# Kernel tuning notes

Hardware: AMD Instinct MI355X
Metric: run time of the kernel (lower is better)

Reference implementation:

```python
import jax, jax.numpy as jnp
import numpy as np

NUM_CLASSES = 80
TOPK = 100
EPS = 1e-6


def _conv(x, w, b, pad):
    y = jax.lax.conv_general_dilated(
        x, w, window_strides=(1, 1), padding=[(pad, pad), (pad, pad)],
        dimension_numbers=('NCHW', 'OIHW', 'NCHW'))
    return y + b[None, :, None, None]


def _seek_local_maximum(p):
    # 8-neighbor local-maximum test with zero padding, plus >= EPS threshold.
    pp = jnp.pad(p, ((0, 0), (0, 0), (1, 1), (1, 1)))
    m = ((p >= pp[:, :, :-2, 1:-1]) & (p >= pp[:, :, 2:, 1:-1]) &
         (p >= pp[:, :, 1:-1, :-2]) & (p >= pp[:, :, 1:-1, 2:]) &
         (p >= pp[:, :, :-2, :-2]) & (p >= pp[:, :, :-2, 2:]) &
         (p >= pp[:, :, 2:, :-2]) & (p >= pp[:, :, 2:, 2:]) &
         (p >= EPS))
    return m.astype(p.dtype)


def setup_inputs() -> dict:
    key = jax.random.key(0)
    k = jax.random.split(key, 4)
    B, C, H, W = 8, 256, 128, 128
    return {
        'x': jax.random.normal(k[0], (B, C, H, W), jnp.float32),
        'pos_embeddings': jax.random.normal(k[1], (1, C, H, W), jnp.float32),
        'w1': jax.random.normal(k[2], (C, C, 3, 3), jnp.float32) * 0.02,
        'b1': jnp.zeros((C,), jnp.float32),
        'w2': jax.random.normal(k[3], (NUM_CLASSES + 1, C, 1, 1), jnp.float32) * 0.02,
        'b2': jnp.zeros((NUM_CLASSES + 1,), jnp.float32),
    }


def reference(x, pos_embeddings, w1, b1, w2, b2):
    b, c, h, w = x.shape
    # conv3x3 -> relu -> conv1x1 class logits  [b, num_classes+1, h, w]
    logits = _conv(jax.nn.relu(_conv(x, w1, b1, 1)), w2, b2, 0)
    probs = jax.nn.softmax(logits, axis=1)
    # keep only the winning foreground class per pixel (one-hot mask)
    cls_idx = jnp.argmax(probs[:, :NUM_CLASSES], axis=1)  # [b, h, w]
    one_hot = jax.nn.one_hot(cls_idx, NUM_CLASSES + 1, dtype=probs.dtype)
    probs = probs * jnp.transpose(one_hot, (0, 3, 1, 2))
    # boost local maxima (unrolled NMS) then topk over best-class score map
    probs = probs + _seek_local_maximum(probs)
    scores = jnp.max(probs[:, :NUM_CLASSES], axis=1).reshape(b, h * w)
    _, idx = jax.lax.top_k(scores, TOPK)  # [b, TOPK]
    topk_proposals = jnp.take_along_axis(
        x.reshape(b, c, h * w), idx[:, None, :], axis=2)
    pe = jnp.broadcast_to(pos_embeddings, (b,) + pos_embeddings.shape[1:])
    topk_pos_embeddings = jnp.take_along_axis(
        pe.reshape(b, -1, h * w), idx[:, None, :], axis=2)
    # eval mode: topk_locations is None in the original; omit it here
    return topk_proposals, topk_pos_embeddings, logits
```

## Files before the change

### kernel.cpp

```cpp
#include <hip/hip_runtime.h>
#include <cmath>

#define BATCH 8
#define CHN 256
#define HH 128
#define WW 128
#define HWSZ (HH*WW)
#define NCLS 81
#define NFG 80
#define KTOP 100
#define EPSV 1e-6f

typedef __attribute__((ext_vector_type(8))) short short8;
typedef __attribute__((ext_vector_type(4))) float f32x4;

__device__ __forceinline__ ushort f2bf(float f) {
    unsigned u = __float_as_uint(f);
    return (ushort)((u + 0x7FFFu + ((u >> 16) & 1u)) >> 16);
}
__device__ __forceinline__ float bf2f(ushort h) {
    return __uint_as_float(((unsigned)h) << 16);
}

__device__ __forceinline__ void gl16(const void* g, void* l) {
    __builtin_amdgcn_global_load_lds(
        (const __attribute__((address_space(1))) void*)g,
        (__attribute__((address_space(3))) void*)l, 16, 0, 0);
}

__global__ __launch_bounds__(256) void prep_x(
    const float* __restrict__ x, ushort* __restrict__ xh, ushort* __restrict__ xl)
{
    __shared__ float tile[32 * 321];
    const int blk = blockIdx.x;
    const int q4 = blk & 3, h = (blk >> 2) & 127, b = blk >> 9;
    const int w0 = q4 << 5;
    const int t = threadIdx.x;
    const int px1 = t & 31, cq = t >> 5;

    const float* xb = x + ((size_t)b * CHN) * HWSZ + h * WW + w0;
#pragma unroll 4
    for (int i = 0; i < 32; ++i) {
        tile[px1 * 321 + i * 10 + cq] = xb[(size_t)(i * 8 + cq) * HWSZ + px1];
    }
    __syncthreads();
    for (int i = 0; i < 4; ++i) {
        int u = i * 256 + t;
        int c8 = u & 31, px = u >> 5;
        short8 hv, lv;
#pragma unroll
        for (int j = 0; j < 8; ++j) {
            float f = tile[px * 321 + c8 * 10 + j];
            ushort hb = f2bf(f);
            hv[j] = (short)hb;
            lv[j] = (short)f2bf(f - bf2f(hb));
        }
        size_t addr = ((size_t)b * HWSZ + h * WW + w0 + px) * CHN + c8 * 8;
        *(short8*)(xh + addr) = hv;
        *(short8*)(xl + addr) = lv;
    }
}

__global__ __launch_bounds__(256) void prep_w(
    const float* __restrict__ w1, const float* __restrict__ w2,
    ushort* __restrict__ Bsw, ushort* __restrict__ w2sw)
{
    int i = blockIdx.x * 256 + threadIdx.x;
    if (i < 73728) {
        int tap  = i >> 13;
        int rem  = i & 8191;
        int kt   = rem >> 10;
        int rem2 = rem & 1023;
        int ntg  = rem2 >> 6;
        int lane = rem2 & 63;
        int oc   = ntg * 16 + (lane & 15);
        int ic0  = kt * 32 + (lane >> 4) * 8;
        size_t base = (size_t)(tap * 8 + kt) * 16384 + (size_t)ntg * 512 + lane * 8;
#pragma unroll
        for (int j = 0; j < 8; ++j) {
            float w  = w1[(size_t)oc * 2304 + (ic0 + j) * 9 + tap];
            ushort hb = f2bf(w);
            Bsw[base + j]        = hb;
            Bsw[base + 8192 + j] = f2bf(w - bf2f(hb));
        }
    } else {
        int j2 = i - 73728;
        int kt   = j2 / 768;
        int rem  = j2 - kt * 768;
        int spl  = rem / 384;
        int rem2 = rem - spl * 384;
        int ntg  = rem2 >> 6;
        int lane = rem2 & 63;
        int oc   = ntg * 16 + (lane & 15);
        int ic0  = kt * 32 + (lane >> 4) * 8;
        size_t base = (size_t)(kt * 12 + spl * 6 + ntg) * 512 + lane * 8;
#pragma unroll
        for (int j = 0; j < 8; ++j) {
            float w = (oc < NCLS) ? w2[(size_t)oc * CHN + ic0 + j] : 0.f;
            ushort hb = f2bf(w);
            w2sw[base + j] = spl ? f2bf(w - bf2f(hb)) : hb;
        }
    }
}

__global__ __launch_bounds__(256, 2) void conv3_pipe(
    const ushort* __restrict__ xh, const ushort* __restrict__ xl,
    const ushort* __restrict__ Bsw, const float* __restrict__ b1,
    float* __restrict__ y)
{
    __shared__ ushort A[3][2][132 * 32];

    const int blk  = blockIdx.x;
    const int b    = blk & 7;
    const int h    = blk >> 3;
    const int t    = threadIdx.x;
    const int lane = t & 63;
    const int w    = t >> 6;
    const int l15  = lane & 15;
    const int q    = lane >> 4;

    int colb[4], basew[4];
#pragma unroll
    for (int r = 0; r < 4; ++r) {
        int e   = (r * 256 + t) & 511;
        int pxs = (e >> 2) + 1;
        int qq  = e & 3;
        int qs  = qq ^ ((pxs >> 1) & 3);
        colb[r]  = (pxs - 1) * CHN + qs * 8;
        basew[r] = ((((r * 256 + (t & 192)) & 511) >> 2) + 1) * 32;
    }

    const short8 zz = {0, 0, 0, 0, 0, 0, 0, 0};
    f32x4 acc[8][4];
#pragma unroll
    for (int i = 0; i < 8; ++i)
#pragma unroll
        for (int j = 0; j < 4; ++j) { f32x4 z = {0.f, 0.f, 0.f, 0.f}; acc[i][j] = z; }

    if (t < 96) {
        int sl = t >> 5, rr = t & 31, arr = rr >> 4, pp = (rr >> 2) & 3, qq = rr & 3;
        int pxs = pp ? 128 + pp : 0;
        *(short8*)&A[sl][arr][pxs * 32 + qq * 8] = zz;
    }
    if (h == 0 || h == 127) {
        const int sl = (h == 0) ? 0 : 2;
        for (int u = t; u < 1056; u += 256) {
            int arr = u >= 528; int v = arr ? u - 528 : u;
            *(short8*)&A[sl][arr][v * 8] = zz;
        }
    }

    auto stage = [&](int sn) {
        int kt1 = sn / 3;
        int kh1 = sn - kt1 * 3;
        int gh  = h - 1 + kh1;
        if ((unsigned)gh < (unsigned)HH) {
            size_t rowb = ((size_t)(b * HH + gh) * WW) * CHN + kt1 * 32;
#pragma unroll
            for (int r = 0; r < 4; ++r) {
                const ushort* g = (r < 2 ? xh : xl) + rowb + colb[r];
                gl16(g, &A[kh1][r >> 1][basew[r]]);
            }
        }
    };

    stage(0);
    stage(1);

#pragma unroll 1
    for (int s = 0; s < 24; ++s) {
        const int kt = s / 3;
        const int kh = s - kt * 3;
        {
            const int kh1n = (s + 1) % 3;
            const bool nx4 = (s < 23) &&
                !((h == 0 && kh1n == 0) || (h == 127 && kh1n == 2));
            if (nx4) asm volatile("s_waitcnt vmcnt(4) lgkmcnt(0)" ::: "memory");
            else     asm volatile("s_waitcnt vmcnt(0) lgkmcnt(0)" ::: "memory");
            __builtin_amdgcn_s_barrier();
            __builtin_amdgcn_sched_barrier(0);
        }
#pragma unroll
        for (int kw = 0; kw < 3; ++kw) {
            const int tap = kh * 3 + kw;
            const ushort* bk = Bsw + (size_t)(tap * 8 + kt) * 16384 + lane * 8;
            short8 bh[4], bl[4];
#pragma unroll
            for (int nt = 0; nt < 4; ++nt) {
                bh[nt] = *(const short8*)(bk + (w * 4 + nt) * 512);
                bl[nt] = *(const short8*)(bk + 8192 + (w * 4 + nt) * 512);
            }
            if (kw == 0 && s < 22) stage(s + 2);
#pragma unroll
            for (int mth = 0; mth < 8; mth += 4) {
                short8 ahf[4], alf[4];
#pragma unroll
                for (int mm = 0; mm < 4; ++mm) {
                    int pxs = (mth + mm) * 16 + l15 + kw;
                    int cof = pxs * 32 + ((q ^ ((pxs >> 1) & 3)) * 8);
                    ahf[mm] = *(const short8*)&A[kh][0][cof];
                    alf[mm] = *(const short8*)&A[kh][1][cof];
                }
                __builtin_amdgcn_s_setprio(1);
#pragma unroll
                for (int nt = 0; nt < 4; ++nt) {
#pragma unroll
                    for (int mm = 0; mm < 4; ++mm)
                        acc[mth + mm][nt] = __builtin_amdgcn_mfma_f32_16x16x32_bf16(
                            ahf[mm], bh[nt], acc[mth + mm][nt], 0, 0, 0);
#pragma unroll
                    for (int mm = 0; mm < 4; ++mm)
                        acc[mth + mm][nt] = __builtin_amdgcn_mfma_f32_16x16x32_bf16(
                            ahf[mm], bl[nt], acc[mth + mm][nt], 0, 0, 0);
#pragma unroll
                    for (int mm = 0; mm < 4; ++mm)
                        acc[mth + mm][nt] = __builtin_amdgcn_mfma_f32_16x16x32_bf16(
                            alf[mm], bh[nt], acc[mth + mm][nt], 0, 0, 0);
                }
                __builtin_amdgcn_s_setprio(0);
            }
        }
    }

    const size_t rowbase = (size_t)b * HWSZ + h * WW;
#pragma unroll
    for (int nt = 0; nt < 4; ++nt) {
        const int oc = w * 64 + nt * 16 + l15;
        const float bias = b1[oc];
#pragma unroll
        for (int mt = 0; mt < 8; ++mt) {
#pragma unroll
            for (int r = 0; r < 4; ++r) {
                const int px = mt * 16 + q * 4 + r;
                float v = acc[mt][nt][r] + bias;
                y[(rowbase + px) * CHN + oc] = v > 0.f ? v : 0.f;
            }
        }
    }
}

__global__ __launch_bounds__(256) void head_mfma(
    const float* __restrict__ y, const ushort* __restrict__ w2sw,
    const float* __restrict__ b2, float* __restrict__ logits_out,
    int* __restrict__ cls_map, float* __restrict__ prob_map)
{
    __shared__ float ls[128][97];
    const int blk = blockIdx.x;
    const int b = blk >> 7, h = blk & 127;
    const int t = threadIdx.x, lane = t & 63, wm = t >> 6;
    const int l15 = lane & 15, q = lane >> 4;

    f32x4 acc[2][6];
#pragma unroll
    for (int i = 0; i < 2; ++i)
#pragma unroll
        for (int j = 0; j < 6; ++j) { f32x4 z = {0.f, 0.f, 0.f, 0.f}; acc[i][j] = z; }

    const size_t rowbase = (size_t)b * HWSZ + h * WW;
    const float* yb0 = y + (rowbase + wm * 32 + l15) * CHN + q * 8;
    const float* yb1 = yb0 + 16 * CHN;

    float4 fa[2][4], fb[2][4];
#pragma unroll
    for (int k = 0; k < 4; ++k) {
        fa[0][k] = *(const float4*)(yb0 + k * 32);
        fb[0][k] = *(const float4*)(yb0 + k * 32 + 4);
        fa[1][k] = *(const float4*)(yb1 + k * 32);
        fb[1][k] = *(const float4*)(yb1 + k * 32 + 4);
    }

#pragma unroll
    for (int kt = 0; kt < 8; ++kt) {
        const int sl = kt & 3;
        short8 ah[2], al[2];
#pragma unroll
        for (int mt = 0; mt < 2; ++mt) {
            float4 f0 = fa[mt][sl];
            float4 f1 = fb[mt][sl];
            float fv[8] = {f0.x, f0.y, f0.z, f0.w, f1.x, f1.y, f1.z, f1.w};
#pragma unroll
            for (int j = 0; j < 8; ++j) {
                ushort hb = f2bf(fv[j]);
                ah[mt][j] = (short)hb;
                al[mt][j] = (short)f2bf(fv[j] - bf2f(hb));
            }
        }
        if (kt < 4) {
            fa[0][sl] = *(const float4*)(yb0 + (kt + 4) * 32);
            fb[0][sl] = *(const float4*)(yb0 + (kt + 4) * 32 + 4);
            fa[1][sl] = *(const float4*)(yb1 + (kt + 4) * 32);
            fb[1][sl] = *(const float4*)(yb1 + (kt + 4) * 32 + 4);
        }
        const ushort* bk = w2sw + (size_t)kt * 12 * 512 + lane * 8;
#pragma unroll
        for (int nt = 0; nt < 6; ++nt) {
            short8 bh = *(const short8*)(bk + nt * 512);
            short8 bl = *(const short8*)(bk + (6 + nt) * 512);
#pragma unroll
            for (int mt = 0; mt < 2; ++mt) {
                acc[mt][nt] = __builtin_amdgcn_mfma_f32_16x16x32_bf16(ah[mt], bh, acc[mt][nt], 0, 0, 0);
                acc[mt][nt] = __builtin_amdgcn_mfma_f32_16x16x32_bf16(ah[mt], bl, acc[mt][nt], 0, 0, 0);
                acc[mt][nt] = __builtin_amdgcn_mfma_f32_16x16x32_bf16(al[mt], bh, acc[mt][nt], 0, 0, 0);
            }
        }
    }

#pragma unroll
    for (int nt = 0; nt < 6; ++nt) {
        const int oc = nt * 16 + l15;
        const float bias = (oc < NCLS) ? b2[oc] : 0.f;
#pragma unroll
        for (int mt = 0; mt < 2; ++mt) {
#pragma unroll
            for (int r = 0; r < 4; ++r) {
                const int px = wm * 32 + mt * 16 + q * 4 + r;
                ls[px][oc] = acc[mt][nt][r] + bias;
            }
        }
    }
    __syncthreads();

    for (int i = t; i < NCLS * 128; i += 256) {
        int c = i >> 7, px = i & 127;
        logits_out[((size_t)b * NCLS + c) * HWSZ + h * WW + px] = ls[px][c];
    }

    if (t < 128) {
        const int px = t;
        float m = -1e30f;
#pragma unroll
        for (int c = 0; c < NCLS; ++c) m = fmaxf(m, ls[px][c]);
        float s = 0.f;
        for (int c = 0; c < NCLS; ++c) s += expf(ls[px][c] - m);
        float best = -1e30f; int bc = 0;
        for (int c = 0; c < NFG; ++c) {
            float v = ls[px][c];
            if (v > best) { best = v; bc = c; }
        }
        cls_map[rowbase + px]  = bc;
        prob_map[rowbase + px] = expf(best - m) / s;
    }
}

__global__ __launch_bounds__(256) void locmax_kernel(
    const int* __restrict__ cls_map, const float* __restrict__ prob_map,
    float* __restrict__ score)
{
    int i = blockIdx.x * 256 + threadIdx.x;
    int b = i >> 14;
    int p = i & (HWSZ - 1);
    int h = p >> 7, w = p & 127;
    int mycls = cls_map[i];
    float myp = prob_map[i];
    bool lm = (myp >= EPSV);
#pragma unroll
    for (int dh = -1; dh <= 1; ++dh)
#pragma unroll
        for (int dw = -1; dw <= 1; ++dw) {
            if (dh == 0 && dw == 0) continue;
            int nh = h + dh, nw = w + dw;
            if ((unsigned)nh < HH && (unsigned)nw < WW) {
                int ni = b * HWSZ + nh * WW + nw;
                if (cls_map[ni] == mycls && myp < prob_map[ni]) lm = false;
            }
        }
    score[i] = myp + (lm ? 1.f : 0.f);
}

__global__ __launch_bounds__(1024) void topk_kernel(
    const float* __restrict__ score, int* __restrict__ idx_out)
{
    __shared__ unsigned int hist[256];
    __shared__ unsigned long long cand[2048];
    __shared__ unsigned int sprefix, sneed, scntA, scntB;
    const int b = blockIdx.x;
    const int t = threadIdx.x;
    const float* sc = score + b * HWSZ;

    unsigned keys[16];
#pragma unroll
    for (int i = 0; i < 16; ++i)
        keys[i] = __float_as_uint(sc[t + (i << 10)]);

    if (t == 0) { sneed = KTOP; sprefix = 0; scntA = 0; scntB = 0; }

    for (int lvl = 0; lvl < 4; ++lvl) {
        const int shift = 24 - 8 * lvl;
        if (t < 256) hist[t] = 0;
        __syncthreads();
        const unsigned pref = sprefix;
#pragma unroll
        for (int i = 0; i < 16; ++i) {
            unsigned k = keys[i];
            bool match = (lvl == 0) || ((k >> (shift + 8)) == pref);
            if (match) atomicAdd(&hist[(k >> shift) & 255u], 1u);
        }
        __syncthreads();
        if (t == 0) {
            unsigned needv = sneed, c = 0; int bsel = 0;
            for (int j = 255; j >= 0; --j) {
                unsigned nc = c + hist[j];
                if (nc >= needv) { bsel = j; break; }
                c = nc;
            }
            sprefix = (pref << 8) | (unsigned)bsel;
            sneed = needv - c;
        }
        __syncthreads();
    }

    const unsigned K = sprefix;
#pragma unroll
    for (int i = 0; i < 16; ++i) {
        unsigned k = keys[i];
        int p = t + (i << 10);
        if (k > K) {
            unsigned pos = atomicAdd(&scntA, 1u);
            cand[pos] = ((unsigned long long)k << 32) | (unsigned)(~p);
        } else if (k == K) {
            unsigned pos = atomicAdd(&scntB, 1u);
            if (pos < 1920u)
                cand[128 + pos] = ((unsigned long long)k << 32) | (unsigned)(~p);
        }
    }
    __syncthreads();
    const int cA = (int)scntA;
    const int cB = (int)(scntB < 1920u ? scntB : 1920u);
    const int Ctot = cA + cB;
    for (int ti = t; ti < Ctot; ti += 1024) {
        unsigned long long my = cand[ti < cA ? ti : 128 + (ti - cA)];
        int rank = 0;
        for (int j = 0; j < Ctot; ++j) {
            unsigned long long o = cand[j < cA ? j : 128 + (j - cA)];
            rank += (o > my) ? 1 : 0;
        }
        if (rank < KTOP)
            idx_out[b * KTOP + rank] =
                (int)(~(unsigned)(my & 0xFFFFFFFFull)) & (HWSZ - 1);
    }
}

__global__ __launch_bounds__(256) void gather_kernel(
    const float* __restrict__ x, const float* __restrict__ pos,
    const int* __restrict__ idx, float* __restrict__ out0,
    float* __restrict__ out1)
{
    int blk = blockIdx.x;
    int b = blk / KTOP;
    int j = blk - b * KTOP;
    int c = threadIdx.x;
    int pix = idx[b * KTOP + j];
    out0[((size_t)b * CHN + c) * KTOP + j] = x[((size_t)b * CHN + c) * HWSZ + pix];
    out1[((size_t)b * CHN + c) * KTOP + j] = pos[(size_t)c * HWSZ + pix];
}

extern "C" void kernel_launch(void* const* d_in, const int* in_sizes, int n_in,
                              void* d_out, int out_size, void* d_ws, size_t ws_size,
                              hipStream_t stream) {
    (void)in_sizes; (void)n_in; (void)out_size; (void)ws_size;
    const float* x   = (const float*)d_in[0];
    const float* pos = (const float*)d_in[1];
    const float* w1  = (const float*)d_in[2];
    const float* b1  = (const float*)d_in[3];
    const float* w2  = (const float*)d_in[4];
    const float* b2  = (const float*)d_in[5];

    float* out0   = (float*)d_out;
    float* out1   = out0 + BATCH * CHN * KTOP;
    float* logits = out1 + BATCH * CHN * KTOP;

    char* ws = (char*)d_ws;
    const size_t NPX = (size_t)BATCH * HWSZ;

    size_t off = 0;
    int*    cls_map  = (int*)(ws + off);    off += NPX * 4;
    float*  prob_map = (float*)(ws + off);  off += NPX * 4;
    float*  score    = (float*)(ws + off);  off += NPX * 4;
    int*    idx      = (int*)(ws + off);    off += 4096;
    ushort* w2sw     = (ushort*)(ws + off); off += (size_t)8 * 12 * 512 * 2;
    ushort* Bsw      = (ushort*)(ws + off); off += (size_t)9 * 8 * 16384 * 2;
    ushort* xh       = (ushort*)(ws + off); off += NPX * CHN * 2;
    ushort* xl       = (ushort*)(ws + off); off += NPX * CHN * 2;
    float*  y        = (float*)(ws + off);  off += NPX * CHN * 4;

    prep_x<<<4096, 256, 0, stream>>>(x, xh, xl);
    prep_w<<<312, 256, 0, stream>>>(w1, w2, Bsw, w2sw);
    conv3_pipe<<<1024, 256, 0, stream>>>(xh, xl, Bsw, b1, y);
    head_mfma<<<1024, 256, 0, stream>>>(y, w2sw, b2, logits, cls_map, prob_map);
    locmax_kernel<<<(int)(NPX / 256), 256, 0, stream>>>(cls_map, prob_map, score);
    topk_kernel<<<BATCH, 1024, 0, stream>>>(score, idx);
    gather_kernel<<<BATCH * KTOP, 256, 0, stream>>>(x, pos, idx, out0, out1);
}
```

Measured before the change: 702.6 us.

## Precompute conv LDS/B addresses, parallelize topk bin scan, remap gather threads

The conv inner loop now uses precomputed per-lane byte offsets for the A-tile LDS reads and B-fragment loads, which removes the per-iteration swizzle arithmetic. The top-k radix select replaces the serial single-thread 256-bin scan with a parallel suffix sum across 256 threads, at the cost of extra barriers. The gather kernel is remapped to one block per (batch, channel) with threads over the top-k indices, so output writes become contiguous. The conv change matters most because conv dominates runtime, and it only saves address ALU work.

```diff
diff --git a/kernel.cpp b/kernel.cpp
--- a/kernel.cpp
+++ b/kernel.cpp
@@ -128,6 +128,13 @@
         int qs  = qq ^ ((pxs >> 1) & 3);
         colb[r]  = (pxs - 1) * CHN + qs * 8;
         basew[r] = ((((r * 256 + (t & 192)) & 511) >> 2) + 1) * 32;
+    }
+
+    int abase[3];
+#pragma unroll
+    for (int kw = 0; kw < 3; ++kw) {
+        int p0 = l15 + kw;
+        abase[kw] = p0 * 64 + ((q ^ ((p0 >> 1) & 3)) << 4);
     }
 
     const short8 zz = {0, 0, 0, 0, 0, 0, 0, 0};
@@ -183,23 +190,25 @@
 #pragma unroll
         for (int kw = 0; kw < 3; ++kw) {
             const int tap = kh * 3 + kw;
-            const ushort* bk = Bsw + (size_t)(tap * 8 + kt) * 16384 + lane * 8;
+            const char* bkh = (const char*)Bsw +
+                ((size_t)(tap * 8 + kt) << 15) + (w << 12) + (lane << 4);
+            const char* bkl = bkh + 16384;
             short8 bh[4], bl[4];
 #pragma unroll
             for (int nt = 0; nt < 4; ++nt) {
-                bh[nt] = *(const short8*)(bk + (w * 4 + nt) * 512);
-                bl[nt] = *(const short8*)(bk + 8192 + (w * 4 + nt) * 512);
+                bh[nt] = *(const short8*)(bkh + nt * 1024);
+                bl[nt] = *(const short8*)(bkl + nt * 1024);
             }
             if (kw == 0 && s < 22) stage(s + 2);
+            const char* pah = (const char*)&A[kh][0][0] + abase[kw];
+            const char* pal = (const char*)&A[kh][1][0] + abase[kw];
 #pragma unroll
             for (int mth = 0; mth < 8; mth += 4) {
                 short8 ahf[4], alf[4];
 #pragma unroll
                 for (int mm = 0; mm < 4; ++mm) {
-                    int pxs = (mth + mm) * 16 + l15 + kw;
-                    int cof = pxs * 32 + ((q ^ ((pxs >> 1) & 3)) * 8);
-                    ahf[mm] = *(const short8*)&A[kh][0][cof];
-                    alf[mm] = *(const short8*)&A[kh][1][cof];
+                    ahf[mm] = *(const short8*)(pah + (mth + mm) * 1024);
+                    alf[mm] = *(const short8*)(pal + (mth + mm) * 1024);
                 }
                 __builtin_amdgcn_s_setprio(1);
 #pragma unroll
@@ -371,6 +380,7 @@
     const float* __restrict__ score, int* __restrict__ idx_out)
 {
     __shared__ unsigned int hist[256];
+    __shared__ unsigned int suf[256];
     __shared__ unsigned long long cand[2048];
     __shared__ unsigned int sprefix, sneed, scntA, scntB;
     const int b = blockIdx.x;
@@ -396,15 +406,25 @@
             if (match) atomicAdd(&hist[(k >> shift) & 255u], 1u);
         }
         __syncthreads();
-        if (t == 0) {
-            unsigned needv = sneed, c = 0; int bsel = 0;
-            for (int j = 255; j >= 0; --j) {
-                unsigned nc = c + hist[j];
-                if (nc >= needv) { bsel = j; break; }
-                c = nc;
-            }
-            sprefix = (pref << 8) | (unsigned)bsel;
-            sneed = needv - c;
+        if (t < 256) suf[t] = hist[t];
+        __syncthreads();
+#pragma unroll
+        for (int st = 1; st < 256; st <<= 1) {
+            unsigned v = 0;
+            if (t < 256 && t + st < 256) v = suf[t + st];
+            __syncthreads();
+            if (t < 256) suf[t] += v;
+            __syncthreads();
+        }
+        const unsigned needv = sneed;
+        __syncthreads();
+        if (t < 256) {
+            unsigned sj  = suf[t];
+            unsigned sj1 = (t == 255) ? 0u : suf[t + 1];
+            if (sj >= needv && sj1 < needv) {
+                sprefix = (pref << 8) | (unsigned)t;
+                sneed   = needv - sj1;
+            }
         }
         __syncthreads();
     }
@@ -440,18 +460,19 @@
     }
 }
 
-__global__ __launch_bounds__(256) void gather_kernel(
+__global__ __launch_bounds__(128) void gather_kernel(
     const float* __restrict__ x, const float* __restrict__ pos,
     const int* __restrict__ idx, float* __restrict__ out0,
     float* __restrict__ out1)
 {
     int blk = blockIdx.x;
-    int b = blk / KTOP;
-    int j = blk - b * KTOP;
-    int c = threadIdx.x;
-    int pix = idx[b * KTOP + j];
-    out0[((size_t)b * CHN + c) * KTOP + j] = x[((size_t)b * CHN + c) * HWSZ + pix];
-    out1[((size_t)b * CHN + c) * KTOP + j] = pos[(size_t)c * HWSZ + pix];
+    int b = blk >> 8, c = blk & 255;
+    int j = threadIdx.x;
+    if (j < KTOP) {
+        int pix = idx[b * KTOP + j];
+        out0[((size_t)b * CHN + c) * KTOP + j] = x[((size_t)b * CHN + c) * HWSZ + pix];
+        out1[((size_t)b * CHN + c) * KTOP + j] = pos[(size_t)c * HWSZ + pix];
+    }
 }
 
 extern "C" void kernel_launch(void* const* d_in, const int* in_sizes, int n_in,
@@ -489,5 +510,5 @@
     head_mfma<<<1024, 256, 0, stream>>>(y, w2sw, b2, logits, cls_map, prob_map);
     locmax_kernel<<<(int)(NPX / 256), 256, 0, stream>>>(cls_map, prob_map, score);
     topk_kernel<<<BATCH, 1024, 0, stream>>>(score, idx);
-    gather_kernel<<<BATCH * KTOP, 256, 0, stream>>>(x, pos, idx, out0, out1);
-}
+    gather_kernel<<<BATCH * CHN, 128, 0, stream>>>(x, pos, idx, out0, out1);
+}
```

Result: faster. 664.4 us (-5.4%).
